# Kernel tuning notes

Hardware: AMD Instinct MI355X
Metric: run time of the kernel (lower is better)

The kernel has to match this reference:

```python
import jax, jax.numpy as jnp
import numpy as np

V, S, E, H, D, L = 32000, 1024, 512, 8, 64, 4
FF = 4 * E
EPS = 1e-5


def setup_inputs() -> dict:
    key = jax.random.key(0)
    ks = jax.random.split(key, 24)
    s = 0.02
    inp = {
        "x": jax.random.randint(ks[0], (2, S), 0, V, dtype=jnp.int32),
        "tok_emb": jax.random.normal(ks[1], (V, E), jnp.float32) * s,
        "pos_emb": jax.random.normal(ks[2], (S, E), jnp.float32) * s,
        "Wq": jax.random.normal(ks[3], (L, H, E, D), jnp.float32) * s,
        "bq": jnp.zeros((L, H, D), jnp.float32),
        "Wk": jax.random.normal(ks[4], (L, H, E, D), jnp.float32) * s,
        "bk": jnp.zeros((L, H, D), jnp.float32),
        "Wv": jax.random.normal(ks[5], (L, H, E, D), jnp.float32) * s,
        "bv": jnp.zeros((L, H, D), jnp.float32),
        "Wo": jax.random.normal(ks[6], (L, H * D, E), jnp.float32) * s,
        "bo": jnp.zeros((L, E), jnp.float32),
        "W1": jax.random.normal(ks[7], (L, E, FF), jnp.float32) * s,
        "b1": jnp.zeros((L, FF), jnp.float32),
        "W2": jax.random.normal(ks[8], (L, FF, E), jnp.float32) * s,
        "b2": jnp.zeros((L, E), jnp.float32),
        "ln1_g": jnp.ones((L, E), jnp.float32),
        "ln1_b": jnp.zeros((L, E), jnp.float32),
        "ln2_g": jnp.ones((L, E), jnp.float32),
        "ln2_b": jnp.zeros((L, E), jnp.float32),
        "Wout": jax.random.normal(ks[9], (E, V), jnp.float32) * s,
        "bout": jnp.zeros((V,), jnp.float32),
    }
    return inp


def _layernorm(x, g, b):
    mu = jnp.mean(x, axis=-1, keepdims=True)
    var = jnp.mean(jnp.square(x - mu), axis=-1, keepdims=True)
    return (x - mu) * jax.lax.rsqrt(var + EPS) * g + b


def _decoder(h, Wq, bq, Wk, bk, Wv, bv, Wo, bo, W1, b1, W2, b2, g1, be1, g2, be2):
    B, T, _ = h.shape
    # per-head Q/K/V projections, batched over heads (matches concat of per-head linears)
    Q = jnp.einsum("bse,hed->bhsd", h, Wq) + bq[None, :, None, :]
    K = jnp.einsum("bse,hed->bhsd", h, Wk) + bk[None, :, None, :]
    Vv = jnp.einsum("bse,hed->bhsd", h, Wv) + bv[None, :, None, :]
    scores = jnp.einsum("bhqd,bhkd->bhqk", Q, K) / jnp.sqrt(jnp.asarray(D, h.dtype))
    causal = jnp.tril(jnp.ones((T, T), bool))
    scores = jnp.where(causal[None, None], scores, -jnp.inf)
    attn = jax.nn.softmax(scores, axis=-1)
    out = jnp.einsum("bhqk,bhkd->bhqd", attn, Vv)
    conc = out.transpose(0, 2, 1, 3).reshape(B, T, H * D)  # concat heads along feature dim
    mha = conc @ Wo + bo
    ln = _layernorm(h + mha, g1, be1)
    ff = jax.nn.relu(ln @ W1 + b1) @ W2 + b2
    return _layernorm(ln + ff, g2, be2)


def reference(x, tok_emb, pos_emb, Wq, bq, Wk, bk, Wv, bv, Wo, bo,
              W1, b1, W2, b2, ln1_g, ln1_b, ln2_g, ln2_b, Wout, bout):
    B, T = x.shape
    h = tok_emb[x] + pos_emb[:T][None]  # [B,T,E]
    for l in range(L):
        h = _decoder(h, Wq[l], bq[l], Wk[l], bk[l], Wv[l], bv[l], Wo[l], bo[l],
                     W1[l], b1[l], W2[l], b2[l], ln1_g[l], ln1_b[l], ln2_g[l], ln2_b[l])
    return h @ Wout + bout  # [B,T,V] logits
```

## Files before the change

kernel.cpp:

```cpp
#include <hip/hip_runtime.h>
#include <hip/hip_bf16.h>


#define B_ 2
#define S_ 1024
#define E_ 512
#define H_ 8
#define D_ 64
#define L_ 4
#define FF_ 2048
#define V_ 32000
#define M_ (B_ * S_)
#define QKV_N (3 * H_ * D_)

typedef __attribute__((ext_vector_type(8))) short short8;
typedef __attribute__((ext_vector_type(4))) float f32x4;

__device__ __forceinline__ float b2f(ushort u) {
  union { uint32_t i; float f; } c; c.i = ((uint32_t)u) << 16; return c.f;
}
__device__ __forceinline__ ushort f2b(float f) {
  union { float f; uint32_t i; } c; c.f = f;
  uint32_t u = c.i;
  return (ushort)((u + 0x7FFFu + ((u >> 16) & 1u)) >> 16);
}

__device__ __forceinline__ void gload16(const ushort* g, ushort* l) {
  __builtin_amdgcn_global_load_lds(
      (const __attribute__((address_space(1))) void*)g,
      (__attribute__((address_space(3))) void*)l, 16, 0, 0);
}

__global__ __launch_bounds__(256) void embed_kernel(
    const int* __restrict__ x, const float* __restrict__ tok,
    const float* __restrict__ pos, float* __restrict__ hf,
    ushort* __restrict__ hb) {
  int idx = blockIdx.x * 256 + threadIdx.x;
  int e = idx & (E_ - 1);
  int t = (idx >> 9) & (S_ - 1);
  int b = idx >> 19;
  int tokid = x[b * S_ + t];
  float v = tok[(size_t)tokid * E_ + e] + pos[(size_t)t * E_ + e];
  hf[idx] = v;
  hb[idx] = f2b(v);
}

__global__ __launch_bounds__(256) void transpose_cvt_kernel(
    const float* __restrict__ in, ushort* __restrict__ out, int R, int C,
    int B2, long long inS1, long long inS2, long long outS1, long long outS2) {
  __shared__ float tile[32][33];
  int bz = blockIdx.z;
  int b1 = bz / B2, b2 = bz % B2;
  in += (size_t)b1 * inS1 + (size_t)b2 * inS2;
  out += (size_t)b1 * outS1 + (size_t)b2 * outS2;
  int r0 = blockIdx.x * 32, c0 = blockIdx.y * 32;
  int tx = threadIdx.x & 31, ty = threadIdx.x >> 5;
#pragma unroll
  for (int i = 0; i < 4; i++)
    tile[ty + 8 * i][tx] = in[(size_t)(r0 + ty + 8 * i) * C + c0 + tx];
  __syncthreads();
#pragma unroll
  for (int i = 0; i < 4; i++)
    out[(size_t)(c0 + ty + 8 * i) * R + r0 + tx] = f2b(tile[tx][ty + 8 * i]);
}

__global__ __launch_bounds__(256) void qkvw_kernel(
    const float* __restrict__ Wq, const float* __restrict__ Wk,
    const float* __restrict__ Wv, ushort* __restrict__ wqkv) {
  __shared__ float tile[32][33];
  int bz = blockIdx.z;
  int t = bz / (L_ * H_);
  int rem = bz % (L_ * H_);
  int lyr = rem / H_, h = rem % H_;
  const float* in = ((t == 0) ? Wq : (t == 1) ? Wk : Wv) +
                    ((size_t)lyr * H_ + h) * E_ * D_;
  ushort* out = wqkv + (size_t)lyr * QKV_N * E_ + ((size_t)t * 512 + h * 64) * E_;
  int r0 = blockIdx.x * 32, c0 = blockIdx.y * 32;
  int tx = threadIdx.x & 31, ty = threadIdx.x >> 5;
#pragma unroll
  for (int i = 0; i < 4; i++)
    tile[ty + 8 * i][tx] = in[(size_t)(r0 + ty + 8 * i) * D_ + c0 + tx];
  __syncthreads();
#pragma unroll
  for (int i = 0; i < 4; i++)
    out[(size_t)(c0 + ty + 8 * i) * E_ + r0 + tx] = f2b(tile[tx][ty + 8 * i]);
}

__global__ __launch_bounds__(256) void pack_b_kernel(
    const float* __restrict__ bq, const float* __restrict__ bk,
    const float* __restrict__ bv, float* __restrict__ bp) {
  int idx = blockIdx.x * 256 + threadIdx.x;
  if (idx >= L_ * QKV_N) return;
  int n = idx % QKV_N;
  int l = idx / QKV_N;
  int t = n / (H_ * D_);
  int hd = n % (H_ * D_);
  const float* src = (t == 0) ? bq : (t == 1) ? bk : bv;
  bp[idx] = src[(size_t)l * H_ * D_ + hd];
}

template <bool OUTBF, bool RELU, bool VT>
__global__ __launch_bounds__(256) void mfma_gemm_kernel(
    const ushort* __restrict__ A, const ushort* __restrict__ Bt,
    const float* __restrict__ bias, const float* __restrict__ resid,
    void* __restrict__ out, ushort* __restrict__ vt,
    int M, int N, int K, int gx) {
  __shared__ __align__(16) ushort As[128 * 64];
  __shared__ __align__(16) ushort Bs[128 * 64];
  int tid = threadIdx.x;
  int w = tid >> 6, l = tid & 63;
  int wr = w >> 1, wc = w & 1;
  int lane15 = l & 15, lhi = l >> 4;

  int bid = blockIdx.x;
  int bx = bid % gx, by = bid / gx;
  int row0 = by * 128, col0 = bx * 128;

  int rr8 = l >> 3;
  int ksrc = (((l & 7) ^ rr8) << 3);
  const ushort *gA[2][2], *gB[2][2];
  ushort *lA[2][2], *lB[2][2];
#pragma unroll
  for (int cc = 0; cc < 2; cc++) {
    int c = w + cc * 4;
#pragma unroll
    for (int h = 0; h < 2; h++) {
      int row = c * 16 + h * 8 + rr8;
      gA[cc][h] = A + (size_t)(row0 + row) * K + ksrc;
      gB[cc][h] = Bt + (size_t)(col0 + row) * K + ksrc;
      int ldst = c * 1024 + h * 512 + l * 8;
      lA[cc][h] = &As[ldst];
      lB[cc][h] = &Bs[ldst];
    }
  }

  f32x4 acc[4][4] = {};

  for (int k0 = 0; k0 < K; k0 += 64) {
#pragma unroll
    for (int cc = 0; cc < 2; cc++)
#pragma unroll
      for (int h = 0; h < 2; h++) {
        gload16(gA[cc][h] + k0, lA[cc][h]);
        gload16(gB[cc][h] + k0, lB[cc][h]);
      }
    __syncthreads();
    short8 a[4][2], b[4][2];
    int sa = (lane15 & 7) << 4;
#pragma unroll
    for (int i = 0; i < 4; i++) {
      int ra = (wr * 64 + i * 16 + lane15) * 64;
      int rb = (wc * 64 + i * 16 + lane15) * 64;
#pragma unroll
      for (int kk = 0; kk < 2; kk++) {
        int inner = ((kk * 64 + lhi * 16) ^ sa) >> 1;
        a[i][kk] = *(const short8*)&As[ra + inner];
        b[i][kk] = *(const short8*)&Bs[rb + inner];
      }
    }
#pragma unroll
    for (int i = 0; i < 4; i++)
#pragma unroll
      for (int j = 0; j < 4; j++) {
        acc[i][j] = __builtin_amdgcn_mfma_f32_16x16x32_bf16(a[i][0], b[j][0], acc[i][j], 0, 0, 0);
        acc[i][j] = __builtin_amdgcn_mfma_f32_16x16x32_bf16(a[i][1], b[j][1], acc[i][j], 0, 0, 0);
      }
    __syncthreads();
  }

  float* outf = (float*)out;
  ushort* outb = (ushort*)out;
#pragma unroll
  for (int i = 0; i < 4; i++) {
    int gr = row0 + wr * 64 + i * 16 + lhi * 4;
#pragma unroll
    for (int j = 0; j < 4; j++) {
      int gc = col0 + wc * 64 + j * 16 + lane15;
      float bb = bias[gc];
#pragma unroll
      for (int r = 0; r < 4; r++) {
        float v = acc[i][j][r] + bb;
        if (resid) v += resid[(size_t)(gr + r) * N + gc];
        if (RELU) v = fmaxf(v, 0.f);
        if (VT && gc >= 1024) {
          int d = gc - 1024;
          int grr = gr + r;
          int bb2 = grr >> 10, s = grr & 1023;
          vt[(((size_t)(bb2 * 8 + (d >> 6)) * 64 + (d & 63)) << 10) + s] = f2b(v);
        } else if (OUTBF) {
          outb[(size_t)(gr + r) * N + gc] = f2b(v);
        } else {
          outf[(size_t)(gr + r) * N + gc] = v;
        }
      }
    }
  }
}

template <int SK>
__global__ __launch_bounds__(256) void mfma_gemm_sk_kernel(
    const ushort* __restrict__ A, const ushort* __restrict__ Bt,
    float* __restrict__ part, int M, int N, int K, int gx) {
  __shared__ __align__(16) ushort As[128 * 64];
  __shared__ __align__(16) ushort Bs[128 * 64];
  int tid = threadIdx.x;
  int w = tid >> 6, l = tid & 63;
  int wr = w >> 1, wc = w & 1;
  int lane15 = l & 15, lhi = l >> 4;

  int tiles = gx * (M >> 7);
  int sk = blockIdx.x / tiles;
  int rem = blockIdx.x % tiles;
  int bx = rem % gx, by = rem / gx;
  int row0 = by * 128, col0 = bx * 128;
  int klen = K / SK, kbeg = sk * klen;

  int rr8 = l >> 3;
  int ksrc = (((l & 7) ^ rr8) << 3);
  const ushort *gA[2][2], *gB[2][2];
  ushort *lA[2][2], *lB[2][2];
#pragma unroll
  for (int cc = 0; cc < 2; cc++) {
    int c = w + cc * 4;
#pragma unroll
    for (int h = 0; h < 2; h++) {
      int row = c * 16 + h * 8 + rr8;
      gA[cc][h] = A + (size_t)(row0 + row) * K + ksrc;
      gB[cc][h] = Bt + (size_t)(col0 + row) * K + ksrc;
      int ldst = c * 1024 + h * 512 + l * 8;
      lA[cc][h] = &As[ldst];
      lB[cc][h] = &Bs[ldst];
    }
  }

  f32x4 acc[4][4] = {};

  for (int k0 = kbeg; k0 < kbeg + klen; k0 += 64) {
#pragma unroll
    for (int cc = 0; cc < 2; cc++)
#pragma unroll
      for (int h = 0; h < 2; h++) {
        gload16(gA[cc][h] + k0, lA[cc][h]);
        gload16(gB[cc][h] + k0, lB[cc][h]);
      }
    __syncthreads();
    short8 a[4][2], b[4][2];
    int sa = (lane15 & 7) << 4;
#pragma unroll
    for (int i = 0; i < 4; i++) {
      int ra = (wr * 64 + i * 16 + lane15) * 64;
      int rb = (wc * 64 + i * 16 + lane15) * 64;
#pragma unroll
      for (int kk = 0; kk < 2; kk++) {
        int inner = ((kk * 64 + lhi * 16) ^ sa) >> 1;
        a[i][kk] = *(const short8*)&As[ra + inner];
        b[i][kk] = *(const short8*)&Bs[rb + inner];
      }
    }
#pragma unroll
    for (int i = 0; i < 4; i++)
#pragma unroll
      for (int j = 0; j < 4; j++) {
        acc[i][j] = __builtin_amdgcn_mfma_f32_16x16x32_bf16(a[i][0], b[j][0], acc[i][j], 0, 0, 0);
        acc[i][j] = __builtin_amdgcn_mfma_f32_16x16x32_bf16(a[i][1], b[j][1], acc[i][j], 0, 0, 0);
      }
    __syncthreads();
  }

  float* dst = part + (size_t)sk * M * N;
#pragma unroll
  for (int i = 0; i < 4; i++) {
    int gr = row0 + wr * 64 + i * 16 + lhi * 4;
#pragma unroll
    for (int j = 0; j < 4; j++) {
      int gc = col0 + wc * 64 + j * 16 + lane15;
#pragma unroll
      for (int r = 0; r < 4; r++)
        dst[(size_t)(gr + r) * N + gc] = acc[i][j][r];
    }
  }
}

__global__ __launch_bounds__(512) void mfma_gemm256_kernel(
    const ushort* __restrict__ A, const ushort* __restrict__ Bt,
    const float* __restrict__ bias, float* __restrict__ out,
    int M, int N, int K) {
  __shared__ __align__(16) ushort As[2][256 * 64];
  __shared__ __align__(16) ushort Bs[2][256 * 64];
  int tid = threadIdx.x;
  int w = tid >> 6, l = tid & 63;
  int wr = w >> 2, wc = w & 3;
  int lane15 = l & 15, lhi = l >> 4;

  int bid = blockIdx.x;
  int wg = (bid & 7) * 125 + (bid >> 3);
  int by = wg & 7, bx = wg >> 3;
  int row0 = by * 256, col0 = bx * 256;

  const ushort* ga[4];
  const ushort* gb[4];
  int lofs[4];
#pragma unroll
  for (int p2 = 0; p2 < 4; p2++) {
    int i = p2 * 512 + tid;
    int row = i >> 3, kg = i & 7;
    int ksrc = ((kg ^ (row & 7)) << 3);
    ga[p2] = A + (size_t)(row0 + row) * K + ksrc;
    gb[p2] = Bt + (size_t)(col0 + row) * K + ksrc;
    lofs[p2] = i * 8;
  }

  f32x4 acc[8][4] = {};

  auto stage = [&](int buf, int k0) {
    ushort* bA = &As[buf][0];
    ushort* bB = &Bs[buf][0];
#pragma unroll
    for (int p2 = 0; p2 < 4; p2++) {
      gload16(ga[p2] + k0, bA + lofs[p2]);
      gload16(gb[p2] + k0, bB + lofs[p2]);
    }
  };
  auto compute = [&](int buf) {
    const ushort* bA = &As[buf][0];
    const ushort* bB = &Bs[buf][0];
    int sa = (lane15 & 7) << 4;
#pragma unroll
    for (int kk = 0; kk < 2; kk++) {
      int inner = ((kk * 64 + lhi * 16) ^ sa) >> 1;
      short8 a[8], b[4];
#pragma unroll
      for (int i = 0; i < 8; i++)
        a[i] = *(const short8*)&bA[(wr * 128 + i * 16 + lane15) * 64 + inner];
#pragma unroll
      for (int j = 0; j < 4; j++)
        b[j] = *(const short8*)&bB[(wc * 64 + j * 16 + lane15) * 64 + inner];
#pragma unroll
      for (int i = 0; i < 8; i++)
#pragma unroll
        for (int j = 0; j < 4; j++)
          acc[i][j] = __builtin_amdgcn_mfma_f32_16x16x32_bf16(a[i], b[j], acc[i][j], 0, 0, 0);
    }
  };

  stage(0, 0);
  __syncthreads();
  int cur = 0;
  int nt = K >> 6;
  for (int t = 0; t < nt - 1; t++) {
    stage(cur ^ 1, (t + 1) << 6);
    compute(cur);
    __syncthreads();
    cur ^= 1;
  }
  compute(cur);

#pragma unroll
  for (int i = 0; i < 8; i++) {
    int gr = row0 + wr * 128 + i * 16 + lhi * 4;
#pragma unroll
    for (int j = 0; j < 4; j++) {
      int gc = col0 + wc * 64 + j * 16 + lane15;
      float bb = bias[gc];
#pragma unroll
      for (int r = 0; r < 4; r++)
        out[(size_t)(gr + r) * N + gc] = acc[i][j][r] + bb;
    }
  }
}

__global__ __launch_bounds__(128) void fattn_kernel(
    const ushort* __restrict__ qkv, const ushort* __restrict__ vt,
    ushort* __restrict__ conc) {
  int qb = blockIdx.x;
  int bh = blockIdx.y;
  int b = bh >> 3, h = bh & 7;
  int w = threadIdx.x >> 6, l = threadIdx.x & 63;
  int lane15 = l & 15, lhi = l >> 4;
  int q0 = qb * 32 + w * 16;

  __shared__ __align__(16) ushort plds[2][16][72];

  const ushort* qr = qkv + (size_t)(b * S_ + q0 + lane15) * QKV_N + h * 64;
  short8 qf0 = *(const short8*)(qr + lhi * 8);
  short8 qf1 = *(const short8*)(qr + 32 + lhi * 8);

  f32x4 o[4] = {};
  float m[4], lsum[4];
#pragma unroll
  for (int r = 0; r < 4; r++) { m[r] = -1e30f; lsum[r] = 0.f; }

  const ushort* kbase = qkv + (size_t)b * S_ * QKV_N + 512 + h * 64;
  const ushort* vbase = vt + (size_t)bh * 64 * S_;
  int qtop = q0 + 15;

  for (int kv0 = 0; kv0 <= qtop; kv0 += 64) {
    float sv[4][4];
#pragma unroll
    for (int t = 0; t < 4; t++) {
      if (kv0 + t * 16 <= qtop) {
        const ushort* kr = kbase + (size_t)(kv0 + t * 16 + lane15) * QKV_N;
        short8 kf0 = *(const short8*)(kr + lhi * 8);
        short8 kf1 = *(const short8*)(kr + 32 + lhi * 8);
        f32x4 s = {};
        s = __builtin_amdgcn_mfma_f32_16x16x32_bf16(qf0, kf0, s, 0, 0, 0);
        s = __builtin_amdgcn_mfma_f32_16x16x32_bf16(qf1, kf1, s, 0, 0, 0);
        int kidx = kv0 + t * 16 + lane15;
#pragma unroll
        for (int r = 0; r < 4; r++) {
          float v = s[r] * 0.125f;
          if (kidx > q0 + lhi * 4 + r) v = -1e30f;
          sv[t][r] = v;
        }
      } else {
#pragma unroll
        for (int r = 0; r < 4; r++) sv[t][r] = -1e30f;
      }
    }
#pragma unroll
    for (int r = 0; r < 4; r++) {
      float rm = fmaxf(fmaxf(sv[0][r], sv[1][r]), fmaxf(sv[2][r], sv[3][r]));
      rm = fmaxf(rm, __shfl_xor(rm, 1));
      rm = fmaxf(rm, __shfl_xor(rm, 2));
      rm = fmaxf(rm, __shfl_xor(rm, 4));
      rm = fmaxf(rm, __shfl_xor(rm, 8));
      float mn = fmaxf(m[r], rm);
      float sc = __expf(m[r] - mn);
      m[r] = mn;
      float rs = 0.f;
#pragma unroll
      for (int t = 0; t < 4; t++) {
        float p = __expf(sv[t][r] - mn);
        plds[w][lhi * 4 + r][t * 16 + lane15] = f2b(p);
        rs += p;
      }
      rs += __shfl_xor(rs, 1);
      rs += __shfl_xor(rs, 2);
      rs += __shfl_xor(rs, 4);
      rs += __shfl_xor(rs, 8);
      lsum[r] = lsum[r] * sc + rs;
#pragma unroll
      for (int n = 0; n < 4; n++) o[n][r] *= sc;
    }
    short8 pa0 = *(const short8*)&plds[w][lane15][lhi * 8];
    short8 pa1 = *(const short8*)&plds[w][lane15][32 + lhi * 8];
#pragma unroll
    for (int n = 0; n < 4; n++) {
      const ushort* vr = vbase + (size_t)(n * 16 + lane15) * S_ + kv0;
      short8 vf0 = *(const short8*)(vr + lhi * 8);
      short8 vf1 = *(const short8*)(vr + 32 + lhi * 8);
      o[n] = __builtin_amdgcn_mfma_f32_16x16x32_bf16(pa0, vf0, o[n], 0, 0, 0);
      o[n] = __builtin_amdgcn_mfma_f32_16x16x32_bf16(pa1, vf1, o[n], 0, 0, 0);
    }
  }
#pragma unroll
  for (int r = 0; r < 4; r++) {
    float inv = 1.f / lsum[r];
    int row = b * S_ + q0 + lhi * 4 + r;
#pragma unroll
    for (int n = 0; n < 4; n++)
      conc[(size_t)row * (H_ * D_) + h * 64 + n * 16 + lane15] = f2b(o[n][r] * inv);
  }
}

template <int SK>
__global__ __launch_bounds__(256) void ln_red_kernel(
    const float* __restrict__ part, const float* __restrict__ bias,
    const float* __restrict__ resid, const float* __restrict__ g,
    const float* __restrict__ bsh, float* __restrict__ outf,
    ushort* __restrict__ outb) {
  int w = threadIdx.x >> 6, l = threadIdx.x & 63;
  int row = blockIdx.x * 4 + w;
  size_t off = (size_t)row * E_ + l * 8;
  float4 r0 = *(const float4*)(resid + off);
  float4 r1 = *(const float4*)(resid + off + 4);
  float4 bb0 = *(const float4*)(bias + l * 8);
  float4 bb1 = *(const float4*)(bias + l * 8 + 4);
  float x[8] = {r0.x + bb0.x, r0.y + bb0.y, r0.z + bb0.z, r0.w + bb0.w,
                r1.x + bb1.x, r1.y + bb1.y, r1.z + bb1.z, r1.w + bb1.w};
#pragma unroll
  for (int s = 0; s < SK; s++) {
    const float* ps = part + (size_t)s * M_ * E_ + off;
    float4 p0 = *(const float4*)ps;
    float4 p1 = *(const float4*)(ps + 4);
    x[0] += p0.x; x[1] += p0.y; x[2] += p0.z; x[3] += p0.w;
    x[4] += p1.x; x[5] += p1.y; x[6] += p1.z; x[7] += p1.w;
  }
  float s = 0.f, q = 0.f;
#pragma unroll
  for (int i = 0; i < 8; i++) { s += x[i]; q += x[i] * x[i]; }
#pragma unroll
  for (int off2 = 1; off2 < 64; off2 <<= 1) {
    s += __shfl_xor(s, off2);
    q += __shfl_xor(q, off2);
  }
  float mu = s * (1.f / 512.f);
  float var = q * (1.f / 512.f) - mu * mu;
  float rs = rsqrtf(var + 1e-5f);
  float4 g0 = *(const float4*)(g + l * 8);
  float4 g1 = *(const float4*)(g + l * 8 + 4);
  float4 b0 = *(const float4*)(bsh + l * 8);
  float4 b1 = *(const float4*)(bsh + l * 8 + 4);
  float gg[8] = {g0.x, g0.y, g0.z, g0.w, g1.x, g1.y, g1.z, g1.w};
  float bbv[8] = {b0.x, b0.y, b0.z, b0.w, b1.x, b1.y, b1.z, b1.w};
  float y[8];
#pragma unroll
  for (int i = 0; i < 8; i++) y[i] = (x[i] - mu) * rs * gg[i] + bbv[i];
  float* of = outf + off;
  *(float4*)of = make_float4(y[0], y[1], y[2], y[3]);
  *(float4*)(of + 4) = make_float4(y[4], y[5], y[6], y[7]);
  ushort4 u0 = {f2b(y[0]), f2b(y[1]), f2b(y[2]), f2b(y[3])};
  ushort4 u1 = {f2b(y[4]), f2b(y[5]), f2b(y[6]), f2b(y[7])};
  ushort* ob = outb + off;
  *(ushort4*)ob = u0;
  *(ushort4*)(ob + 4) = u1;
}

extern "C" void kernel_launch(void* const* d_in, const int* in_sizes, int n_in,
                              void* d_out, int out_size, void* d_ws, size_t ws_size,
                              hipStream_t stream) {
  const int* x = (const int*)d_in[0];
  const float* tok = (const float*)d_in[1];
  const float* pos = (const float*)d_in[2];
  const float* Wq = (const float*)d_in[3];
  const float* bq = (const float*)d_in[4];
  const float* Wk = (const float*)d_in[5];
  const float* bk = (const float*)d_in[6];
  const float* Wv = (const float*)d_in[7];
  const float* bv = (const float*)d_in[8];
  const float* Wo = (const float*)d_in[9];
  const float* bo = (const float*)d_in[10];
  const float* W1 = (const float*)d_in[11];
  const float* b1 = (const float*)d_in[12];
  const float* W2 = (const float*)d_in[13];
  const float* b2 = (const float*)d_in[14];
  const float* ln1g = (const float*)d_in[15];
  const float* ln1b = (const float*)d_in[16];
  const float* ln2g = (const float*)d_in[17];
  const float* ln2b = (const float*)d_in[18];
  const float* Wout = (const float*)d_in[19];
  const float* bout = (const float*)d_in[20];
  float* out = (float*)d_out;

  char* p = (char*)d_ws;
  auto alloc = [&](size_t bytes) {
    char* r = p;
    p += (bytes + 255) & ~(size_t)255;
    return r;
  };
  float* h_f = (float*)alloc((size_t)M_ * E_ * 4);
  ushort* h_b = (ushort*)alloc((size_t)M_ * E_ * 2);
  ushort* qkv_b = (ushort*)alloc((size_t)M_ * QKV_N * 2);
  ushort* conc_b = (ushort*)alloc((size_t)M_ * E_ * 2);
  float* part = (float*)alloc((size_t)4 * M_ * E_ * 4);
  float* ln_f = (float*)alloc((size_t)M_ * E_ * 4);
  ushort* ln_b = (ushort*)alloc((size_t)M_ * E_ * 2);
  ushort* ff_b = (ushort*)alloc((size_t)M_ * FF_ * 2);
  ushort* vt_b = (ushort*)alloc((size_t)B_ * H_ * D_ * S_ * 2);
  ushort* wqkv = (ushort*)alloc((size_t)L_ * QKV_N * E_ * 2);
  float* bqkv = (float*)alloc((size_t)L_ * QKV_N * 4);
  ushort* wo_t = (ushort*)alloc((size_t)L_ * E_ * E_ * 2);
  ushort* w1_t = (ushort*)alloc((size_t)L_ * FF_ * E_ * 2);
  ushort* w2_t = (ushort*)alloc((size_t)L_ * E_ * FF_ * 2);
  ushort* wout_t = (ushort*)alloc((size_t)V_ * E_ * 2);

  qkvw_kernel<<<dim3(E_ / 32, D_ / 32, 3 * L_ * H_), 256, 0, stream>>>(Wq, Wk, Wv, wqkv);
  transpose_cvt_kernel<<<dim3(16, 16, L_), 256, 0, stream>>>(
      Wo, wo_t, 512, 512, 1, (long long)512 * 512, 0, (long long)512 * 512, 0);
  transpose_cvt_kernel<<<dim3(E_ / 32, FF_ / 32, L_), 256, 0, stream>>>(
      W1, w1_t, E_, FF_, 1, (long long)E_ * FF_, 0, (long long)FF_ * E_, 0);
  transpose_cvt_kernel<<<dim3(FF_ / 32, E_ / 32, L_), 256, 0, stream>>>(
      W2, w2_t, FF_, E_, 1, (long long)FF_ * E_, 0, (long long)E_ * FF_, 0);
  transpose_cvt_kernel<<<dim3(E_ / 32, V_ / 32, 1), 256, 0, stream>>>(
      Wout, wout_t, E_, V_, 1, 0, 0, 0, 0);
  pack_b_kernel<<<(L_ * QKV_N + 255) / 256, 256, 0, stream>>>(bq, bk, bv, bqkv);

  embed_kernel<<<(M_ * E_) / 256, 256, 0, stream>>>(x, tok, pos, h_f, h_b);

  for (int l = 0; l < L_; ++l) {
    mfma_gemm_kernel<true, false, true><<<(QKV_N / 128) * (M_ / 128), 256, 0, stream>>>(
        h_b, wqkv + (size_t)l * QKV_N * E_, bqkv + l * QKV_N, nullptr,
        qkv_b, vt_b, M_, QKV_N, E_, QKV_N / 128);
    fattn_kernel<<<dim3(S_ / 32, B_ * H_), 128, 0, stream>>>(qkv_b, vt_b, conc_b);
    mfma_gemm_sk_kernel<4><<<4 * (E_ / 128) * (M_ / 128), 256, 0, stream>>>(
        conc_b, wo_t + (size_t)l * E_ * E_, part, M_, E_, E_, E_ / 128);
    ln_red_kernel<4><<<M_ / 4, 256, 0, stream>>>(
        part, bo + l * E_, h_f, ln1g + l * E_, ln1b + l * E_, ln_f, ln_b);
    mfma_gemm_kernel<true, true, false><<<(FF_ / 128) * (M_ / 128), 256, 0, stream>>>(
        ln_b, w1_t + (size_t)l * FF_ * E_, b1 + l * FF_, nullptr, ff_b, nullptr,
        M_, FF_, E_, FF_ / 128);
    mfma_gemm_sk_kernel<4><<<4 * (E_ / 128) * (M_ / 128), 256, 0, stream>>>(
        ff_b, w2_t + (size_t)l * E_ * FF_, part, M_, E_, FF_, E_ / 128);
    ln_red_kernel<4><<<M_ / 4, 256, 0, stream>>>(
        part, b2 + l * E_, ln_f, ln2g + l * E_, ln2b + l * E_, h_f, h_b);
  }

  mfma_gemm256_kernel<<<(M_ / 256) * (V_ / 256), 512, 0, stream>>>(
      h_b, wout_t, bout, out, M_, V_, E_);
}
```

Baseline: 651.9 us.

## Fuse setup kernels into one launch and retile final vocab GEMM with deeper pipeline

The six weight-transpose, bias-pack and embedding kernels are merged into a single setup kernel that dispatches on block index, removing several launches and their gaps. The final logits GEMM moves from 256x256 tiles to 128x256 tiles, which doubles the block count to improve occupancy and balance. It also gives B a triple buffer, replaces the plain syncthreads loop with explicit vmcnt waits and raw s_barriers, and raises wave priority around the MFMA section. The hand-written waitcnt values are fragile: if the count of outstanding loads is wrong, the kernel reads shared memory that has not arrived yet.

```diff
diff --git a/kernel.cpp b/kernel.cpp
--- a/kernel.cpp
+++ b/kernel.cpp
@@ -31,72 +31,80 @@
       (__attribute__((address_space(3))) void*)l, 16, 0, 0);
 }
 
-__global__ __launch_bounds__(256) void embed_kernel(
+__global__ __launch_bounds__(256) void setup_kernel(
     const int* __restrict__ x, const float* __restrict__ tok,
-    const float* __restrict__ pos, float* __restrict__ hf,
-    ushort* __restrict__ hb) {
-  int idx = blockIdx.x * 256 + threadIdx.x;
-  int e = idx & (E_ - 1);
-  int t = (idx >> 9) & (S_ - 1);
-  int b = idx >> 19;
-  int tokid = x[b * S_ + t];
-  float v = tok[(size_t)tokid * E_ + e] + pos[(size_t)t * E_ + e];
-  hf[idx] = v;
-  hb[idx] = f2b(v);
-}
-
-__global__ __launch_bounds__(256) void transpose_cvt_kernel(
-    const float* __restrict__ in, ushort* __restrict__ out, int R, int C,
-    int B2, long long inS1, long long inS2, long long outS1, long long outS2) {
+    const float* __restrict__ pos, float* __restrict__ hf, ushort* __restrict__ hb,
+    const float* __restrict__ Wq, const float* __restrict__ Wk,
+    const float* __restrict__ Wv, ushort* __restrict__ wqkv,
+    const float* __restrict__ Wo, ushort* __restrict__ wo_t,
+    const float* __restrict__ W1, ushort* __restrict__ w1_t,
+    const float* __restrict__ W2, ushort* __restrict__ w2_t,
+    const float* __restrict__ Wout, ushort* __restrict__ wout_t,
+    const float* __restrict__ bq, const float* __restrict__ bk,
+    const float* __restrict__ bv, float* __restrict__ bqkv) {
   __shared__ float tile[32][33];
-  int bz = blockIdx.z;
-  int b1 = bz / B2, b2 = bz % B2;
-  in += (size_t)b1 * inS1 + (size_t)b2 * inS2;
-  out += (size_t)b1 * outS1 + (size_t)b2 * outS2;
-  int r0 = blockIdx.x * 32, c0 = blockIdx.y * 32;
-  int tx = threadIdx.x & 31, ty = threadIdx.x >> 5;
-#pragma unroll
-  for (int i = 0; i < 4; i++)
-    tile[ty + 8 * i][tx] = in[(size_t)(r0 + ty + 8 * i) * C + c0 + tx];
-  __syncthreads();
-#pragma unroll
-  for (int i = 0; i < 4; i++)
-    out[(size_t)(c0 + ty + 8 * i) * R + r0 + tx] = f2b(tile[tx][ty + 8 * i]);
-}
-
-__global__ __launch_bounds__(256) void qkvw_kernel(
-    const float* __restrict__ Wq, const float* __restrict__ Wk,
-    const float* __restrict__ Wv, ushort* __restrict__ wqkv) {
-  __shared__ float tile[32][33];
-  int bz = blockIdx.z;
-  int t = bz / (L_ * H_);
-  int rem = bz % (L_ * H_);
-  int lyr = rem / H_, h = rem % H_;
-  const float* in = ((t == 0) ? Wq : (t == 1) ? Wk : Wv) +
-                    ((size_t)lyr * H_ + h) * E_ * D_;
-  ushort* out = wqkv + (size_t)lyr * QKV_N * E_ + ((size_t)t * 512 + h * 64) * E_;
-  int r0 = blockIdx.x * 32, c0 = blockIdx.y * 32;
-  int tx = threadIdx.x & 31, ty = threadIdx.x >> 5;
-#pragma unroll
-  for (int i = 0; i < 4; i++)
-    tile[ty + 8 * i][tx] = in[(size_t)(r0 + ty + 8 * i) * D_ + c0 + tx];
-  __syncthreads();
-#pragma unroll
-  for (int i = 0; i < 4; i++)
-    out[(size_t)(c0 + ty + 8 * i) * E_ + r0 + tx] = f2b(tile[tx][ty + 8 * i]);
-}
-
-__global__ __launch_bounds__(256) void pack_b_kernel(
-    const float* __restrict__ bq, const float* __restrict__ bk,
-    const float* __restrict__ bv, float* __restrict__ bp) {
-  int idx = blockIdx.x * 256 + threadIdx.x;
-  if (idx >= L_ * QKV_N) return;
-  int n = idx % QKV_N;
-  int l = idx / QKV_N;
-  int t = n / (H_ * D_);
-  int hd = n % (H_ * D_);
-  const float* src = (t == 0) ? bq : (t == 1) ? bk : bv;
-  bp[idx] = src[(size_t)l * H_ * D_ + hd];
+  int bz = blockIdx.x;
+  int tid = threadIdx.x;
+
+  auto tr32 = [&](const float* in, ushort* out, int inC, int R, int r0, int c0) {
+    int tx = tid & 31, ty = tid >> 5;
+#pragma unroll
+    for (int i = 0; i < 4; i++)
+      tile[ty + 8 * i][tx] = in[(size_t)(r0 + ty + 8 * i) * inC + c0 + tx];
+    __syncthreads();
+#pragma unroll
+    for (int i = 0; i < 4; i++)
+      out[(size_t)(c0 + ty + 8 * i) * R + r0 + tx] = f2b(tile[tx][ty + 8 * i]);
+  };
+
+  if (bz < 4096) {
+    int idx = bz * 256 + tid;
+    int e = idx & (E_ - 1);
+    int t = (idx >> 9) & (S_ - 1);
+    int b = idx >> 19;
+    int tokid = x[b * S_ + t];
+    float v = tok[(size_t)tokid * E_ + e] + pos[(size_t)t * E_ + e];
+    hf[idx] = v;
+    hb[idx] = f2b(v);
+  } else if (bz < 7168) {
+    int li = bz - 4096;
+    int batch = li >> 5, q = li & 31;
+    int t = batch / (L_ * H_);
+    int rem = batch % (L_ * H_);
+    int lyr = rem / H_, h = rem % H_;
+    const float* in = ((t == 0) ? Wq : (t == 1) ? Wk : Wv) +
+                      ((size_t)lyr * H_ + h) * E_ * D_;
+    ushort* out = wqkv + (size_t)lyr * QKV_N * E_ + ((size_t)t * 512 + h * 64) * E_;
+    tr32(in, out, D_, E_, (q & 15) * 32, (q >> 4) * 32);
+  } else if (bz < 8192) {
+    int li = bz - 7168;
+    int lyr = li >> 8, q = li & 255;
+    tr32(Wo + (size_t)lyr * E_ * E_, wo_t + (size_t)lyr * E_ * E_, E_, E_,
+         (q & 15) * 32, (q >> 4) * 32);
+  } else if (bz < 12288) {
+    int li = bz - 8192;
+    int lyr = li >> 10, q = li & 1023;
+    tr32(W1 + (size_t)lyr * E_ * FF_, w1_t + (size_t)lyr * FF_ * E_, FF_, E_,
+         (q & 15) * 32, (q >> 4) * 32);
+  } else if (bz < 16384) {
+    int li = bz - 12288;
+    int lyr = li >> 10, q = li & 1023;
+    tr32(W2 + (size_t)lyr * FF_ * E_, w2_t + (size_t)lyr * E_ * FF_, E_, FF_,
+         (q & 63) * 32, (q >> 6) * 32);
+  } else if (bz < 32384) {
+    int li = bz - 16384;
+    tr32(Wout, wout_t, V_, E_, (li & 15) * 32, (li >> 4) * 32);
+  } else {
+    int idx = (bz - 32384) * 256 + tid;
+    if (idx < L_ * QKV_N) {
+      int n = idx % QKV_N;
+      int lyr = idx / QKV_N;
+      int t = n / (H_ * D_);
+      int hd = n % (H_ * D_);
+      const float* src = (t == 0) ? bq : (t == 1) ? bk : bv;
+      bqkv[idx] = src[(size_t)lyr * H_ * D_ + hd];
+    }
+  }
 }
 
 template <bool OUTBF, bool RELU, bool VT>
@@ -281,83 +289,98 @@
   }
 }
 
-__global__ __launch_bounds__(512) void mfma_gemm256_kernel(
+__global__ __launch_bounds__(512) void gemm_fin_kernel(
     const ushort* __restrict__ A, const ushort* __restrict__ Bt,
-    const float* __restrict__ bias, float* __restrict__ out,
-    int M, int N, int K) {
-  __shared__ __align__(16) ushort As[2][256 * 64];
-  __shared__ __align__(16) ushort Bs[2][256 * 64];
+    const float* __restrict__ bias, float* __restrict__ out) {
+  constexpr int K = E_, N = V_, NT = E_ / 64;
+  __shared__ __align__(16) ushort As[2][128 * 64];
+  __shared__ __align__(16) ushort Bs[3][256 * 64];
   int tid = threadIdx.x;
   int w = tid >> 6, l = tid & 63;
   int wr = w >> 2, wc = w & 3;
   int lane15 = l & 15, lhi = l >> 4;
 
   int bid = blockIdx.x;
-  int wg = (bid & 7) * 125 + (bid >> 3);
-  int by = wg & 7, bx = wg >> 3;
-  int row0 = by * 256, col0 = bx * 256;
-
-  const ushort* ga[4];
-  const ushort* gb[4];
-  int lofs[4];
-#pragma unroll
-  for (int p2 = 0; p2 < 4; p2++) {
-    int i = p2 * 512 + tid;
+  int wg = (bid & 7) * 250 + (bid >> 3);
+  int by = wg & 15, bx = wg >> 4;
+  int row0 = by * 128, col0 = bx * 256;
+
+  const ushort* ga[2]; int la[2];
+  const ushort* gb[4]; int lb[4];
+#pragma unroll
+  for (int p = 0; p < 2; p++) {
+    int i = p * 512 + tid;
     int row = i >> 3, kg = i & 7;
-    int ksrc = ((kg ^ (row & 7)) << 3);
-    ga[p2] = A + (size_t)(row0 + row) * K + ksrc;
-    gb[p2] = Bt + (size_t)(col0 + row) * K + ksrc;
-    lofs[p2] = i * 8;
-  }
-
-  f32x4 acc[8][4] = {};
-
-  auto stage = [&](int buf, int k0) {
-    ushort* bA = &As[buf][0];
-    ushort* bB = &Bs[buf][0];
-#pragma unroll
-    for (int p2 = 0; p2 < 4; p2++) {
-      gload16(ga[p2] + k0, bA + lofs[p2]);
-      gload16(gb[p2] + k0, bB + lofs[p2]);
-    }
+    ga[p] = A + (size_t)(row0 + row) * K + ((kg ^ (row & 7)) << 3);
+    la[p] = i * 8;
+  }
+#pragma unroll
+  for (int p = 0; p < 4; p++) {
+    int i = p * 512 + tid;
+    int row = i >> 3, kg = i & 7;
+    gb[p] = Bt + (size_t)(col0 + row) * K + ((kg ^ (row & 7)) << 3);
+    lb[p] = i * 8;
+  }
+
+  f32x4 acc[4][4] = {};
+
+  auto stageA = [&](int buf, int t) {
+    int k0 = t << 6;
+#pragma unroll
+    for (int p = 0; p < 2; p++) gload16(ga[p] + k0, &As[buf][la[p]]);
   };
-  auto compute = [&](int buf) {
-    const ushort* bA = &As[buf][0];
-    const ushort* bB = &Bs[buf][0];
+  auto stageB = [&](int buf, int t) {
+    int k0 = t << 6;
+#pragma unroll
+    for (int p = 0; p < 4; p++) gload16(gb[p] + k0, &Bs[buf][lb[p]]);
+  };
+  auto compute = [&](int ba, int bb) {
     int sa = (lane15 & 7) << 4;
 #pragma unroll
     for (int kk = 0; kk < 2; kk++) {
       int inner = ((kk * 64 + lhi * 16) ^ sa) >> 1;
-      short8 a[8], b[4];
-#pragma unroll
-      for (int i = 0; i < 8; i++)
-        a[i] = *(const short8*)&bA[(wr * 128 + i * 16 + lane15) * 64 + inner];
+      short8 a[4], b[4];
+#pragma unroll
+      for (int i = 0; i < 4; i++)
+        a[i] = *(const short8*)&As[ba][(wr * 64 + i * 16 + lane15) * 64 + inner];
 #pragma unroll
       for (int j = 0; j < 4; j++)
-        b[j] = *(const short8*)&bB[(wc * 64 + j * 16 + lane15) * 64 + inner];
-#pragma unroll
-      for (int i = 0; i < 8; i++)
+        b[j] = *(const short8*)&Bs[bb][(wc * 64 + j * 16 + lane15) * 64 + inner];
+#pragma unroll
+      for (int i = 0; i < 4; i++)
 #pragma unroll
         for (int j = 0; j < 4; j++)
           acc[i][j] = __builtin_amdgcn_mfma_f32_16x16x32_bf16(a[i], b[j], acc[i][j], 0, 0, 0);
     }
   };
 
-  stage(0, 0);
-  __syncthreads();
-  int cur = 0;
-  int nt = K >> 6;
-  for (int t = 0; t < nt - 1; t++) {
-    stage(cur ^ 1, (t + 1) << 6);
-    compute(cur);
-    __syncthreads();
-    cur ^= 1;
-  }
-  compute(cur);
-
-#pragma unroll
-  for (int i = 0; i < 8; i++) {
-    int gr = row0 + wr * 128 + i * 16 + lhi * 4;
+  stageA(0, 0);
+  stageB(0, 0);
+  stageB(1, 1);
+  __builtin_amdgcn_sched_barrier(0);
+  asm volatile("s_waitcnt vmcnt(4)" ::: "memory");
+  __builtin_amdgcn_s_barrier();
+  __builtin_amdgcn_sched_barrier(0);
+
+#pragma unroll
+  for (int t = 0; t < NT; t++) {
+    if (t + 1 < NT) stageA((t + 1) & 1, t + 1);
+    if (t + 2 < NT) stageB((t + 2) % 3, t + 2);
+    __builtin_amdgcn_s_setprio(1);
+    compute(t & 1, t % 3);
+    __builtin_amdgcn_s_setprio(0);
+    if (t + 1 < NT) {
+      __builtin_amdgcn_sched_barrier(0);
+      if (t + 2 < NT) asm volatile("s_waitcnt vmcnt(4)" ::: "memory");
+      else            asm volatile("s_waitcnt vmcnt(0)" ::: "memory");
+      __builtin_amdgcn_s_barrier();
+      __builtin_amdgcn_sched_barrier(0);
+    }
+  }
+
+#pragma unroll
+  for (int i = 0; i < 4; i++) {
+    int gr = row0 + wr * 64 + i * 16 + lhi * 4;
 #pragma unroll
     for (int j = 0; j < 4; j++) {
       int gc = col0 + wc * 64 + j * 16 + lane15;
@@ -564,18 +587,9 @@
   ushort* w2_t = (ushort*)alloc((size_t)L_ * E_ * FF_ * 2);
   ushort* wout_t = (ushort*)alloc((size_t)V_ * E_ * 2);
 
-  qkvw_kernel<<<dim3(E_ / 32, D_ / 32, 3 * L_ * H_), 256, 0, stream>>>(Wq, Wk, Wv, wqkv);
-  transpose_cvt_kernel<<<dim3(16, 16, L_), 256, 0, stream>>>(
-      Wo, wo_t, 512, 512, 1, (long long)512 * 512, 0, (long long)512 * 512, 0);
-  transpose_cvt_kernel<<<dim3(E_ / 32, FF_ / 32, L_), 256, 0, stream>>>(
-      W1, w1_t, E_, FF_, 1, (long long)E_ * FF_, 0, (long long)FF_ * E_, 0);
-  transpose_cvt_kernel<<<dim3(FF_ / 32, E_ / 32, L_), 256, 0, stream>>>(
-      W2, w2_t, FF_, E_, 1, (long long)FF_ * E_, 0, (long long)E_ * FF_, 0);
-  transpose_cvt_kernel<<<dim3(E_ / 32, V_ / 32, 1), 256, 0, stream>>>(
-      Wout, wout_t, E_, V_, 1, 0, 0, 0, 0);
-  pack_b_kernel<<<(L_ * QKV_N + 255) / 256, 256, 0, stream>>>(bq, bk, bv, bqkv);
-
-  embed_kernel<<<(M_ * E_) / 256, 256, 0, stream>>>(x, tok, pos, h_f, h_b);
+  setup_kernel<<<32408, 256, 0, stream>>>(
+      x, tok, pos, h_f, h_b, Wq, Wk, Wv, wqkv, Wo, wo_t, W1, w1_t,
+      W2, w2_t, Wout, wout_t, bq, bk, bv, bqkv);
 
   for (int l = 0; l < L_; ++l) {
     mfma_gemm_kernel<true, false, true><<<(QKV_N / 128) * (M_ / 128), 256, 0, stream>>>(
@@ -595,6 +609,6 @@
         part, b2 + l * E_, ln_f, ln2g + l * E_, ln2b + l * E_, h_f, h_b);
   }
 
-  mfma_gemm256_kernel<<<(M_ / 256) * (V_ / 256), 512, 0, stream>>>(
-      h_b, wout_t, bout, out, M_, V_, E_);
-}
+  gemm_fin_kernel<<<(M_ / 128) * (V_ / 256), 512, 0, stream>>>(
+      h_b, wout_t, bout, out);
+}
```

Result: no change. 653.8 us (+0.3%).
